# Performance work log

Measured on AMD Instinct MI355X. Metric: run time of the kernel, lower is better.

The kernel has to match this reference:

```python
import jax, jax.numpy as jnp
import numpy as np

N_NODES = 100000
N_EDGES = 1600000
D_FEAT = 128
N_CLASS = 40
K_HOPS = 2  # nlayers


def setup_inputs() -> dict:
    key = jax.random.key(0)
    k1, k2, k3, k4, k5 = jax.random.split(key, 5)
    src = jax.random.randint(k1, (N_EDGES,), 0, N_NODES)
    dst = jax.random.randint(k2, (N_EDGES,), 0, N_NODES)
    features = jax.random.normal(k3, (N_NODES, D_FEAT), dtype=jnp.float32)
    # positive edge weights (EdgeWeightNorm requires nonnegative)
    edge_weight = jax.random.uniform(k4, (N_EDGES,), dtype=jnp.float32, minval=0.1, maxval=1.0)
    W = jax.random.normal(k5, (D_FEAT, N_CLASS), dtype=jnp.float32) / np.float32(np.sqrt(D_FEAT))
    b = jnp.zeros((N_CLASS,), dtype=jnp.float32)
    return {"features": features, "src": src, "dst": dst,
            "edge_weight": edge_weight, "W": W, "b": b}


def reference(features, src, dst, edge_weight, W, b):
    """SGConv (DGL) with edge_weight: EdgeWeightNorm('both') then k SpMM hops, then fc."""
    n = features.shape[0]
    # EdgeWeightNorm('both'): w_ij / sqrt(out_deg_w(src_i) * in_deg_w(dst_j))
    out_deg = jax.ops.segment_sum(edge_weight, src, num_segments=n)  # weighted out-degree
    in_deg = jax.ops.segment_sum(edge_weight, dst, num_segments=n)   # weighted in-degree
    w = edge_weight * jax.lax.rsqrt(out_deg[src]) * jax.lax.rsqrt(in_deg[dst])  # [E]
    h = features
    for _ in range(K_HOPS):
        # message = h[src] * w ; aggregate = scatter-sum over dst
        h = jax.ops.segment_sum(h[src] * w[:, None], dst, num_segments=n)  # [N, D]
    return h @ W + b  # fc projection [N, C]
```

## Files before the change

### kernel.cpp

```cpp
#include <hip/hip_runtime.h>

#define N_NODES 100000
#define N_EDGES 1600000
#define D_FEAT  128
#define N_CLASS 40
#define ELL_CAP 48

#define QS  10239.6875f
#define DQ  9.765923e-5f
#define FSC  2048.0f
#define FINV (1.0f/2048.0f)
#define CNT_SHIFT 20
#define W_MASK ((1u << CNT_SHIFT) - 1u)

#define RSZ 16000
#define NR 7
#define SLICES 32
#define EPS (N_EDGES/SLICES)
#define HB (NR*SLICES)

#define GEMM_T (N_NODES*(N_CLASS/4))
#define GEMM_B ((GEMM_T + 1023)/1024)

#define NCH 5

__device__ __forceinline__ float bf_lo(unsigned int u) { return __uint_as_float(u << 16); }
__device__ __forceinline__ float bf_hi(unsigned int u) { return __uint_as_float(u & 0xFFFF0000u); }
__device__ __forceinline__ unsigned int bf_pack2(float a, float b) {
    unsigned int ua = __float_as_uint(a), ub = __float_as_uint(b);
    ua = (ua + 0x7FFFu + ((ua >> 16) & 1u)) >> 16;
    ub = (ub + 0x7FFFu + ((ub >> 16) & 1u)) & 0xFFFF0000u;
    return ua | ub;
}

__global__ __launch_bounds__(1024) void mega1_kernel(
    const int* __restrict__ src, const int* __restrict__ dst, const float* __restrict__ ew,
    const float* __restrict__ f, const float* __restrict__ W,
    unsigned int* __restrict__ dhist, unsigned int* __restrict__ shist,
    unsigned int* __restrict__ g0)
{
    __shared__ unsigned int smem[16384];
    const int b = blockIdx.x;
    const int tid = threadIdx.x;

    if (b < 2 * HB) {
        const bool isDst = (b < HB);
        const int b2 = isDst ? b : b - HB;
        const int* idxarr = isDst ? dst : src;
        unsigned int* outh = isDst ? dhist : shist;
        int r = b2 / SLICES, s = b2 - r * SLICES;
        int nb = r * RSZ;
        unsigned int lim = (unsigned int)min(RSZ, N_NODES - nb);
        for (int i = tid; i < RSZ; i += 1024) smem[i] = 0u;
        __syncthreads();
        int e0 = s * EPS;
        const int2*  idx2 = (const int2*)(idxarr + e0);
        const float2* ew2 = (const float2*)(ew + e0);
        const unsigned int cbit = isDst ? (1u << CNT_SHIFT) : 0u;
        for (int i = tid; i < EPS / 2; i += 1024) {
            int2 ii = idx2[i];
            float2 ww = ew2[i];
            unsigned int r0 = (unsigned int)(ii.x - nb);
            unsigned int r1 = (unsigned int)(ii.y - nb);
            if (r0 < lim) atomicAdd(&smem[r0], cbit | (unsigned int)(ww.x * FSC + 0.5f));
            if (r1 < lim) atomicAdd(&smem[r1], cbit | (unsigned int)(ww.y * FSC + 0.5f));
        }
        __syncthreads();
        unsigned int* o = outh + (size_t)b2 * RSZ;
        for (int i = tid; i < RSZ; i += 1024) o[i] = smem[i];
    } else {
        float* Ws = (float*)smem;
        for (int i = tid; i < D_FEAT * N_CLASS; i += 1024) Ws[i] = W[i];
        __syncthreads();
        int idx = (b - 2 * HB) * 1024 + tid;
        if (idx >= GEMM_T) return;
        int n = idx / (N_CLASS / 4);
        int c4 = (idx - n * (N_CLASS / 4)) * 4;
        const float* fr = f + (size_t)n * D_FEAT;
        float4 acc = {0.f, 0.f, 0.f, 0.f};
#pragma unroll 1
        for (int kq = 0; kq < D_FEAT; kq += 4) {
            float4 fv = *(const float4*)(fr + kq);
#pragma unroll
            for (int j = 0; j < 4; ++j) {
                float fs = (j == 0) ? fv.x : (j == 1) ? fv.y : (j == 2) ? fv.z : fv.w;
                const float4 wv = *(const float4*)&Ws[(kq + j) * N_CLASS + c4];
                acc.x = fmaf(fs, wv.x, acc.x);
                acc.y = fmaf(fs, wv.y, acc.y);
                acc.z = fmaf(fs, wv.z, acc.z);
                acc.w = fmaf(fs, wv.w, acc.w);
            }
        }
        uint2 p;
        p.x = bf_pack2(acc.x, acc.y);
        p.y = bf_pack2(acc.z, acc.w);
        *(uint2*)&g0[((size_t)n * N_CLASS + c4) / 2] = p;
    }
}

__global__ void scan_kernel(const unsigned int* __restrict__ dhist,
                            const unsigned int* __restrict__ shist,
                            unsigned char* __restrict__ base8, int* __restrict__ cnt,
                            float* __restrict__ rs_out, float* __restrict__ rs_in)
{
    int n = blockIdx.x * 256 + threadIdx.x;
    if (n >= N_NODES) return;
    int r = n / RSZ, off = n - r * RSZ;
    const unsigned int* dp = dhist + (size_t)r * SLICES * RSZ + off;
    const unsigned int* sp = shist + (size_t)r * SLICES * RSZ + off;
    unsigned char* b8 = base8 + (size_t)r * SLICES * RSZ + off;
    unsigned int ow = 0, iw = 0, run = 0;
#pragma unroll
    for (int s = 0; s < SLICES; ++s) {
        unsigned int dv = dp[(size_t)s * RSZ];
        ow += sp[(size_t)s * RSZ];
        b8[(size_t)s * RSZ] = (unsigned char)run;
        run += dv >> CNT_SHIFT;
        iw += dv & W_MASK;
    }
    rs_out[n] = ow ? rsqrtf((float)ow * FINV) : 0.f;
    rs_in[n]  = iw ? rsqrtf((float)iw * FINV) : 0.f;
    cnt[n] = (int)run;
}

__global__ __launch_bounds__(1024) void fill_kernel(
    const int* __restrict__ src, const int* __restrict__ dst, const float* __restrict__ ew,
    const unsigned char* __restrict__ base8, const float* __restrict__ rs_out,
    unsigned int* __restrict__ ell)
{
    __shared__ unsigned int lds[RSZ];
    const int b = blockIdx.x;
    const int tid = threadIdx.x;
    int r = b / SLICES, s = b - r * SLICES;
    int nb = r * RSZ;
    unsigned int lim = (unsigned int)min(RSZ, N_NODES - nb);
    const unsigned int* bp = (const unsigned int*)(base8 + (size_t)b * RSZ);
    for (int i = tid; i < RSZ / 4; i += 1024) {
        unsigned int v = bp[i];
        lds[4 * i]     = v & 255u;
        lds[4 * i + 1] = (v >> 8) & 255u;
        lds[4 * i + 2] = (v >> 16) & 255u;
        lds[4 * i + 3] = v >> 24;
    }
    __syncthreads();
    int e0 = s * EPS;
    const int2*  d2  = (const int2*)(dst + e0);
    const int2*  s2  = (const int2*)(src + e0);
    const float2* w2 = (const float2*)(ew + e0);
    for (int i = tid; i < EPS / 2; i += 1024) {
        int2 dd = d2[i];
        int2 ss = s2[i];
        float2 ww = w2[i];
#pragma unroll
        for (int j = 0; j < 2; ++j) {
            int d  = (j == 0) ? dd.x : dd.y;
            int sn = (j == 0) ? ss.x : ss.y;
            float w = (j == 0) ? ww.x : ww.y;
            unsigned int rr = (unsigned int)(d - nb);
            if (rr < lim) {
                unsigned int slot = atomicAdd(&lds[rr], 1u);
                if (slot < ELL_CAP) {
                    int q = (int)(w * rs_out[sn] * QS + 0.5f);
                    q = q > 32767 ? 32767 : q;
                    ell[(size_t)d * ELL_CAP + slot] = ((unsigned int)sn << 15) | (unsigned int)q;
                }
            }
        }
    }
}

__global__ void hop_kernel(const unsigned int* __restrict__ ell, const int* __restrict__ cnt,
                           const float* __restrict__ rs_in, const unsigned int* __restrict__ gin,
                           void* __restrict__ gout, const float* __restrict__ bias)
{
    int t = blockIdx.x * 256 + threadIdx.x;
    if (t >= N_NODES * NCH) return;
    int n = t / NCH;
    int c8 = t - n * NCH;
    int k = min(cnt[n], ELL_CAP);
    const uint4* row4 = (const uint4*)(ell + (size_t)n * ELL_CAP);
    const uint4* gin4 = (const uint4*)gin;
    float a0 = 0.f, a1 = 0.f, a2 = 0.f, a3 = 0.f, a4 = 0.f, a5 = 0.f, a6 = 0.f, a7 = 0.f;
    for (int i = 0; i < k; i += 4) {
        uint4 v = row4[i >> 2];
#pragma unroll
        for (int j = 0; j < 4; ++j) {
            if (i + j < k) {
                unsigned int e = (j == 0) ? v.x : (j == 1) ? v.y : (j == 2) ? v.z : v.w;
                float w = (float)(e & 32767u) * DQ;
                uint4 gv = gin4[(size_t)(e >> 15) * NCH + c8];
                a0 = fmaf(w, bf_lo(gv.x), a0); a1 = fmaf(w, bf_hi(gv.x), a1);
                a2 = fmaf(w, bf_lo(gv.y), a2); a3 = fmaf(w, bf_hi(gv.y), a3);
                a4 = fmaf(w, bf_lo(gv.z), a4); a5 = fmaf(w, bf_hi(gv.z), a5);
                a6 = fmaf(w, bf_lo(gv.w), a6); a7 = fmaf(w, bf_hi(gv.w), a7);
            }
        }
    }
    float sc = rs_in[n];
    a0 *= sc; a1 *= sc; a2 *= sc; a3 *= sc; a4 *= sc; a5 *= sc; a6 *= sc; a7 *= sc;
    if (bias) {
        const float4 b0 = *(const float4*)&bias[c8 * 8];
        const float4 b1 = *(const float4*)&bias[c8 * 8 + 4];
        float4 o0 = {a0 + b0.x, a1 + b0.y, a2 + b0.z, a3 + b0.w};
        float4 o1 = {a4 + b1.x, a5 + b1.y, a6 + b1.z, a7 + b1.w};
        float* op = (float*)gout + (size_t)n * N_CLASS + c8 * 8;
        *(float4*)op = o0;
        *(float4*)(op + 4) = o1;
    } else {
        uint4 p;
        p.x = bf_pack2(a0, a1);
        p.y = bf_pack2(a2, a3);
        p.z = bf_pack2(a4, a5);
        p.w = bf_pack2(a6, a7);
        ((uint4*)gout)[(size_t)n * NCH + c8] = p;
    }
}

extern "C" void kernel_launch(void* const* d_in, const int* in_sizes, int n_in,
                              void* d_out, int out_size, void* d_ws, size_t ws_size,
                              hipStream_t stream) {
    const float* features = (const float*)d_in[0];
    const int*   src      = (const int*)d_in[1];
    const int*   dst      = (const int*)d_in[2];
    const float* ew       = (const float*)d_in[3];
    const float* W        = (const float*)d_in[4];
    const float* b        = (const float*)d_in[5];
    float*       out      = (float*)d_out;

    char* ws = (char*)d_ws;
    unsigned int* dhist = (unsigned int*)ws;  ws += (size_t)HB * RSZ * 4;
    unsigned int* shist = (unsigned int*)ws;  ws += (size_t)HB * RSZ * 4;
    unsigned char* base8 = (unsigned char*)ws; ws += (size_t)HB * RSZ;
    int*   cnt    = (int*)ws;    ws += (size_t)N_NODES * 4;
    float* rs_out = (float*)ws;  ws += (size_t)N_NODES * 4;
    float* rs_in  = (float*)ws;  ws += (size_t)N_NODES * 4;
    unsigned int* ell = (unsigned int*)ws; ws += (size_t)N_NODES * ELL_CAP * 4;
    unsigned int* g0  = (unsigned int*)ws;
    unsigned int* g1  = dhist;

    const int B = 256;

    mega1_kernel<<<2 * HB + GEMM_B, 1024, 0, stream>>>(
        src, dst, ew, features, W, dhist, shist, g0);
    scan_kernel<<<(N_NODES + B - 1) / B, B, 0, stream>>>(
        dhist, shist, base8, cnt, rs_out, rs_in);
    fill_kernel<<<HB, 1024, 0, stream>>>(src, dst, ew, base8, rs_out, ell);

    const int HOP_BLOCKS = (N_NODES * NCH + B - 1) / B;
    hop_kernel<<<HOP_BLOCKS, B, 0, stream>>>(ell, cnt, rs_in, g0, (void*)g1, nullptr);
    hop_kernel<<<HOP_BLOCKS, B, 0, stream>>>(ell, cnt, rs_in, g1, (void*)out, b);
}
```

Before: 269.1 us.

## Move feature GEMM into ELL fill kernel, register-block two rows, pad ELL rows

The dense feature projection moves out of the histogram kernel and is co-scheduled with the ELL fill kernel, so the GEMM overlaps the atomic-heavy fill instead of the histogram pass. Each GEMM thread now computes two node rows, reusing each shared-memory weight load across both. The scan kernel zero-pads ELL rows up to a multiple of four so the hop kernel can drop its per-edge bounds check. The trade-offs are a smaller shared array in the histogram kernel, extra padding writes in scan, and a different load balance between the two phases.

Result: slower. 280.9 us (+4.4%).

```diff
diff --git a/kernel.cpp b/kernel.cpp
--- a/kernel.cpp
+++ b/kernel.cpp
@@ -19,8 +19,8 @@
 #define EPS (N_EDGES/SLICES)
 #define HB (NR*SLICES)
 
-#define GEMM_T (N_NODES*(N_CLASS/4))
-#define GEMM_B ((GEMM_T + 1023)/1024)
+#define GEMM2_T ((N_NODES/2)*(N_CLASS/4))
+#define GEMM2_B ((GEMM2_T + 1023)/1024)
 
 #define NCH 5
 
@@ -35,73 +35,42 @@
 
 __global__ __launch_bounds__(1024) void mega1_kernel(
     const int* __restrict__ src, const int* __restrict__ dst, const float* __restrict__ ew,
-    const float* __restrict__ f, const float* __restrict__ W,
-    unsigned int* __restrict__ dhist, unsigned int* __restrict__ shist,
-    unsigned int* __restrict__ g0)
-{
-    __shared__ unsigned int smem[16384];
+    unsigned int* __restrict__ dhist, unsigned int* __restrict__ shist)
+{
+    __shared__ unsigned int smem[RSZ];
     const int b = blockIdx.x;
     const int tid = threadIdx.x;
-
-    if (b < 2 * HB) {
-        const bool isDst = (b < HB);
-        const int b2 = isDst ? b : b - HB;
-        const int* idxarr = isDst ? dst : src;
-        unsigned int* outh = isDst ? dhist : shist;
-        int r = b2 / SLICES, s = b2 - r * SLICES;
-        int nb = r * RSZ;
-        unsigned int lim = (unsigned int)min(RSZ, N_NODES - nb);
-        for (int i = tid; i < RSZ; i += 1024) smem[i] = 0u;
-        __syncthreads();
-        int e0 = s * EPS;
-        const int2*  idx2 = (const int2*)(idxarr + e0);
-        const float2* ew2 = (const float2*)(ew + e0);
-        const unsigned int cbit = isDst ? (1u << CNT_SHIFT) : 0u;
-        for (int i = tid; i < EPS / 2; i += 1024) {
-            int2 ii = idx2[i];
-            float2 ww = ew2[i];
-            unsigned int r0 = (unsigned int)(ii.x - nb);
-            unsigned int r1 = (unsigned int)(ii.y - nb);
-            if (r0 < lim) atomicAdd(&smem[r0], cbit | (unsigned int)(ww.x * FSC + 0.5f));
-            if (r1 < lim) atomicAdd(&smem[r1], cbit | (unsigned int)(ww.y * FSC + 0.5f));
-        }
-        __syncthreads();
-        unsigned int* o = outh + (size_t)b2 * RSZ;
-        for (int i = tid; i < RSZ; i += 1024) o[i] = smem[i];
-    } else {
-        float* Ws = (float*)smem;
-        for (int i = tid; i < D_FEAT * N_CLASS; i += 1024) Ws[i] = W[i];
-        __syncthreads();
-        int idx = (b - 2 * HB) * 1024 + tid;
-        if (idx >= GEMM_T) return;
-        int n = idx / (N_CLASS / 4);
-        int c4 = (idx - n * (N_CLASS / 4)) * 4;
-        const float* fr = f + (size_t)n * D_FEAT;
-        float4 acc = {0.f, 0.f, 0.f, 0.f};
-#pragma unroll 1
-        for (int kq = 0; kq < D_FEAT; kq += 4) {
-            float4 fv = *(const float4*)(fr + kq);
-#pragma unroll
-            for (int j = 0; j < 4; ++j) {
-                float fs = (j == 0) ? fv.x : (j == 1) ? fv.y : (j == 2) ? fv.z : fv.w;
-                const float4 wv = *(const float4*)&Ws[(kq + j) * N_CLASS + c4];
-                acc.x = fmaf(fs, wv.x, acc.x);
-                acc.y = fmaf(fs, wv.y, acc.y);
-                acc.z = fmaf(fs, wv.z, acc.z);
-                acc.w = fmaf(fs, wv.w, acc.w);
-            }
-        }
-        uint2 p;
-        p.x = bf_pack2(acc.x, acc.y);
-        p.y = bf_pack2(acc.z, acc.w);
-        *(uint2*)&g0[((size_t)n * N_CLASS + c4) / 2] = p;
-    }
+    const bool isDst = (b < HB);
+    const int b2 = isDst ? b : b - HB;
+    const int* idxarr = isDst ? dst : src;
+    unsigned int* outh = isDst ? dhist : shist;
+    int r = b2 / SLICES, s = b2 - r * SLICES;
+    int nb = r * RSZ;
+    unsigned int lim = (unsigned int)min(RSZ, N_NODES - nb);
+    for (int i = tid; i < RSZ; i += 1024) smem[i] = 0u;
+    __syncthreads();
+    int e0 = s * EPS;
+    const int2*  idx2 = (const int2*)(idxarr + e0);
+    const float2* ew2 = (const float2*)(ew + e0);
+    const unsigned int cbit = isDst ? (1u << CNT_SHIFT) : 0u;
+    for (int i = tid; i < EPS / 2; i += 1024) {
+        int2 ii = idx2[i];
+        float2 ww = ew2[i];
+        unsigned int r0 = (unsigned int)(ii.x - nb);
+        unsigned int r1 = (unsigned int)(ii.y - nb);
+        if (r0 < lim) atomicAdd(&smem[r0], cbit | (unsigned int)(ww.x * FSC + 0.5f));
+        if (r1 < lim) atomicAdd(&smem[r1], cbit | (unsigned int)(ww.y * FSC + 0.5f));
+    }
+    __syncthreads();
+    unsigned int* o = outh + (size_t)b2 * RSZ;
+    for (int i = tid; i < RSZ; i += 1024) o[i] = smem[i];
 }
 
 __global__ void scan_kernel(const unsigned int* __restrict__ dhist,
                             const unsigned int* __restrict__ shist,
                             unsigned char* __restrict__ base8, int* __restrict__ cnt,
-                            float* __restrict__ rs_out, float* __restrict__ rs_in)
+                            float* __restrict__ rs_out, float* __restrict__ rs_in,
+                            unsigned int* __restrict__ ell)
 {
     int n = blockIdx.x * 256 + threadIdx.x;
     if (n >= N_NODES) return;
@@ -121,51 +90,93 @@
     rs_out[n] = ow ? rsqrtf((float)ow * FINV) : 0.f;
     rs_in[n]  = iw ? rsqrtf((float)iw * FINV) : 0.f;
     cnt[n] = (int)run;
-}
-
-__global__ __launch_bounds__(1024) void fill_kernel(
+    int k  = min((int)run, ELL_CAP);
+    int k4 = min((k + 3) & ~3, ELL_CAP);
+    unsigned int* row = ell + (size_t)n * ELL_CAP;
+    for (int i = k; i < k4; ++i) row[i] = 0u;
+}
+
+__global__ __launch_bounds__(1024) void mega3_kernel(
     const int* __restrict__ src, const int* __restrict__ dst, const float* __restrict__ ew,
     const unsigned char* __restrict__ base8, const float* __restrict__ rs_out,
-    unsigned int* __restrict__ ell)
-{
-    __shared__ unsigned int lds[RSZ];
+    unsigned int* __restrict__ ell,
+    const float* __restrict__ f, const float* __restrict__ W, unsigned int* __restrict__ g0)
+{
+    __shared__ unsigned int smem[RSZ];
     const int b = blockIdx.x;
     const int tid = threadIdx.x;
-    int r = b / SLICES, s = b - r * SLICES;
-    int nb = r * RSZ;
-    unsigned int lim = (unsigned int)min(RSZ, N_NODES - nb);
-    const unsigned int* bp = (const unsigned int*)(base8 + (size_t)b * RSZ);
-    for (int i = tid; i < RSZ / 4; i += 1024) {
-        unsigned int v = bp[i];
-        lds[4 * i]     = v & 255u;
-        lds[4 * i + 1] = (v >> 8) & 255u;
-        lds[4 * i + 2] = (v >> 16) & 255u;
-        lds[4 * i + 3] = v >> 24;
-    }
-    __syncthreads();
-    int e0 = s * EPS;
-    const int2*  d2  = (const int2*)(dst + e0);
-    const int2*  s2  = (const int2*)(src + e0);
-    const float2* w2 = (const float2*)(ew + e0);
-    for (int i = tid; i < EPS / 2; i += 1024) {
-        int2 dd = d2[i];
-        int2 ss = s2[i];
-        float2 ww = w2[i];
-#pragma unroll
-        for (int j = 0; j < 2; ++j) {
-            int d  = (j == 0) ? dd.x : dd.y;
-            int sn = (j == 0) ? ss.x : ss.y;
-            float w = (j == 0) ? ww.x : ww.y;
-            unsigned int rr = (unsigned int)(d - nb);
-            if (rr < lim) {
-                unsigned int slot = atomicAdd(&lds[rr], 1u);
-                if (slot < ELL_CAP) {
-                    int q = (int)(w * rs_out[sn] * QS + 0.5f);
-                    q = q > 32767 ? 32767 : q;
-                    ell[(size_t)d * ELL_CAP + slot] = ((unsigned int)sn << 15) | (unsigned int)q;
+    if (b < HB) {
+        unsigned int* lds = smem;
+        int r = b / SLICES, s = b - r * SLICES;
+        int nb = r * RSZ;
+        unsigned int lim = (unsigned int)min(RSZ, N_NODES - nb);
+        const unsigned int* bp = (const unsigned int*)(base8 + (size_t)b * RSZ);
+        for (int i = tid; i < RSZ / 4; i += 1024) {
+            unsigned int v = bp[i];
+            lds[4 * i]     = v & 255u;
+            lds[4 * i + 1] = (v >> 8) & 255u;
+            lds[4 * i + 2] = (v >> 16) & 255u;
+            lds[4 * i + 3] = v >> 24;
+        }
+        __syncthreads();
+        int e0 = s * EPS;
+        const int2*  d2  = (const int2*)(dst + e0);
+        const int2*  s2  = (const int2*)(src + e0);
+        const float2* w2 = (const float2*)(ew + e0);
+        for (int i = tid; i < EPS / 2; i += 1024) {
+            int2 dd = d2[i];
+            int2 ss = s2[i];
+            float2 ww = w2[i];
+#pragma unroll
+            for (int j = 0; j < 2; ++j) {
+                int d  = (j == 0) ? dd.x : dd.y;
+                int sn = (j == 0) ? ss.x : ss.y;
+                float w = (j == 0) ? ww.x : ww.y;
+                unsigned int rr = (unsigned int)(d - nb);
+                if (rr < lim) {
+                    unsigned int slot = atomicAdd(&lds[rr], 1u);
+                    if (slot < ELL_CAP) {
+                        int q = (int)(w * rs_out[sn] * QS + 0.5f);
+                        q = q > 32767 ? 32767 : q;
+                        ell[(size_t)d * ELL_CAP + slot] = ((unsigned int)sn << 15) | (unsigned int)q;
+                    }
                 }
             }
         }
+    } else {
+        float* Ws = (float*)smem;
+        for (int i = tid; i < D_FEAT * N_CLASS; i += 1024) Ws[i] = W[i];
+        __syncthreads();
+        int idx = (b - HB) * 1024 + tid;
+        if (idx >= GEMM2_T) return;
+        int n2 = idx / (N_CLASS / 4);
+        int c4i = idx - n2 * (N_CLASS / 4);
+        int c4 = c4i * 4;
+        int n0 = n2 * 2;
+        const float* fr0 = f + (size_t)n0 * D_FEAT;
+        const float* fr1 = fr0 + D_FEAT;
+        float4 acc0 = {0.f, 0.f, 0.f, 0.f};
+        float4 acc1 = {0.f, 0.f, 0.f, 0.f};
+#pragma unroll 1
+        for (int kq = 0; kq < D_FEAT; kq += 4) {
+            float4 fv0 = *(const float4*)(fr0 + kq);
+            float4 fv1 = *(const float4*)(fr1 + kq);
+#pragma unroll
+            for (int j = 0; j < 4; ++j) {
+                float fa = (j == 0) ? fv0.x : (j == 1) ? fv0.y : (j == 2) ? fv0.z : fv0.w;
+                float fb = (j == 0) ? fv1.x : (j == 1) ? fv1.y : (j == 2) ? fv1.z : fv1.w;
+                const float4 wv = *(const float4*)&Ws[(kq + j) * N_CLASS + c4];
+                acc0.x = fmaf(fa, wv.x, acc0.x); acc0.y = fmaf(fa, wv.y, acc0.y);
+                acc0.z = fmaf(fa, wv.z, acc0.z); acc0.w = fmaf(fa, wv.w, acc0.w);
+                acc1.x = fmaf(fb, wv.x, acc1.x); acc1.y = fmaf(fb, wv.y, acc1.y);
+                acc1.z = fmaf(fb, wv.z, acc1.z); acc1.w = fmaf(fb, wv.w, acc1.w);
+            }
+        }
+        uint2 p0, p1;
+        p0.x = bf_pack2(acc0.x, acc0.y); p0.y = bf_pack2(acc0.z, acc0.w);
+        p1.x = bf_pack2(acc1.x, acc1.y); p1.y = bf_pack2(acc1.z, acc1.w);
+        *(uint2*)&g0[(size_t)n0 * (N_CLASS / 2) + c4i * 2] = p0;
+        *(uint2*)&g0[(size_t)(n0 + 1) * (N_CLASS / 2) + c4i * 2] = p1;
     }
 }
 
@@ -178,6 +189,7 @@
     int n = t / NCH;
     int c8 = t - n * NCH;
     int k = min(cnt[n], ELL_CAP);
+    k = (k + 3) & ~3;
     const uint4* row4 = (const uint4*)(ell + (size_t)n * ELL_CAP);
     const uint4* gin4 = (const uint4*)gin;
     float a0 = 0.f, a1 = 0.f, a2 = 0.f, a3 = 0.f, a4 = 0.f, a5 = 0.f, a6 = 0.f, a7 = 0.f;
@@ -185,15 +197,13 @@
         uint4 v = row4[i >> 2];
 #pragma unroll
         for (int j = 0; j < 4; ++j) {
-            if (i + j < k) {
-                unsigned int e = (j == 0) ? v.x : (j == 1) ? v.y : (j == 2) ? v.z : v.w;
-                float w = (float)(e & 32767u) * DQ;
-                uint4 gv = gin4[(size_t)(e >> 15) * NCH + c8];
-                a0 = fmaf(w, bf_lo(gv.x), a0); a1 = fmaf(w, bf_hi(gv.x), a1);
-                a2 = fmaf(w, bf_lo(gv.y), a2); a3 = fmaf(w, bf_hi(gv.y), a3);
-                a4 = fmaf(w, bf_lo(gv.z), a4); a5 = fmaf(w, bf_hi(gv.z), a5);
-                a6 = fmaf(w, bf_lo(gv.w), a6); a7 = fmaf(w, bf_hi(gv.w), a7);
-            }
+            unsigned int e = (j == 0) ? v.x : (j == 1) ? v.y : (j == 2) ? v.z : v.w;
+            float w = (float)(e & 32767u) * DQ;
+            uint4 gv = gin4[(size_t)(e >> 15) * NCH + c8];
+            a0 = fmaf(w, bf_lo(gv.x), a0); a1 = fmaf(w, bf_hi(gv.x), a1);
+            a2 = fmaf(w, bf_lo(gv.y), a2); a3 = fmaf(w, bf_hi(gv.y), a3);
+            a4 = fmaf(w, bf_lo(gv.z), a4); a5 = fmaf(w, bf_hi(gv.z), a5);
+            a6 = fmaf(w, bf_lo(gv.w), a6); a7 = fmaf(w, bf_hi(gv.w), a7);
         }
     }
     float sc = rs_in[n];
@@ -240,11 +250,11 @@
 
     const int B = 256;
 
-    mega1_kernel<<<2 * HB + GEMM_B, 1024, 0, stream>>>(
-        src, dst, ew, features, W, dhist, shist, g0);
+    mega1_kernel<<<2 * HB, 1024, 0, stream>>>(src, dst, ew, dhist, shist);
     scan_kernel<<<(N_NODES + B - 1) / B, B, 0, stream>>>(
-        dhist, shist, base8, cnt, rs_out, rs_in);
-    fill_kernel<<<HB, 1024, 0, stream>>>(src, dst, ew, base8, rs_out, ell);
+        dhist, shist, base8, cnt, rs_out, rs_in, ell);
+    mega3_kernel<<<HB + GEMM2_B, 1024, 0, stream>>>(
+        src, dst, ew, base8, rs_out, ell, features, W, g0);
 
     const int HOP_BLOCKS = (N_NODES * NCH + B - 1) / B;
     hop_kernel<<<HOP_BLOCKS, B, 0, stream>>>(ell, cnt, rs_in, g0, (void*)g1, nullptr);
```
